# Kernel optimization log

Hardware: AMD Instinct MI355X
Metric: run time of the kernel (lower is better)

The kernel has to match this reference:

```python
import jax, jax.numpy as jnp
import numpy as np

EPS = 1e-5
B, C, N = 2, 256, 65536


def conv1x1(x, W, b):
    # Conv1d with kernel_size=1: (B,Cin,N) x (Cout,Cin) -> (B,Cout,N)
    return jnp.einsum('oc,bcn->bon', W, x) + b[None, :, None]


def instance_norm(x):
    # InstanceNorm1d, affine=False, biased variance over the spatial dim
    m = jnp.mean(x, axis=-1, keepdims=True)
    v = jnp.var(x, axis=-1, keepdims=True)
    return (x - m) * jax.lax.rsqrt(v + EPS)


def mesh_conv(x, gemm, W, b):
    # MeshCNN MeshConv: gather self + 4 one-ring neighbor edges, symmetric fns, (1,5) conv.
    Bb, Cc, E = x.shape
    xp = jnp.concatenate([jnp.zeros((Bb, Cc, 1), x.dtype), x], axis=2)  # pad slot 0 (for -1/missing)
    eid = jnp.broadcast_to(jnp.arange(E, dtype=gemm.dtype)[None, :, None], (Bb, E, 1))
    Gi = jnp.concatenate([eid, gemm], axis=2) + 1                      # (B,E,5), +1 shift for pad row
    xt = xp.transpose(0, 2, 1)                                          # (B,E+1,C)
    f = jax.vmap(lambda xb, gb: xb[gb])(xt, Gi)                         # (B,E,5,C) gather
    f = f.transpose(0, 3, 1, 2)                                         # (B,C,E,5)
    f0, f1, f2, f3, f4 = (f[..., i] for i in range(5))
    g = jnp.stack([f0, f1 + f3, f2 + f4, jnp.abs(f1 - f3), jnp.abs(f2 - f4)], axis=-1)
    # Conv2d(Cin,Cout,(1,5)) over (B,C,E,5) -> (B,Cout,E)
    return jnp.einsum('ock,bcek->boe', W, g) + b[None, :, None]


def setup_inputs() -> dict:
    key = jax.random.key(0)
    ks = jax.random.split(key, 20)
    s = 0.05
    inp = {
        'x_0': jax.random.normal(ks[0], (B, C, N), jnp.float32),
        'x_1': jax.random.normal(ks[1], (B, C, N), jnp.float32),
        'gemm': jax.random.randint(ks[2], (B, N, 4), 0, N, jnp.int32),
        # conv_a / conv_b: C -> C//4
        'Wa': jax.random.normal(ks[3], (C // 4, C), jnp.float32) * s,
        'ba': jax.random.normal(ks[4], (C // 4,), jnp.float32) * s,
        'Wb': jax.random.normal(ks[5], (C // 4, C), jnp.float32) * s,
        'bb': jax.random.normal(ks[6], (C // 4,), jnp.float32) * s,
        # conv_a_local / conv_b_local: C//2 -> C//2
        'Wal': jax.random.normal(ks[7], (C // 2, C // 2), jnp.float32) * s,
        'bal': jax.random.normal(ks[8], (C // 2,), jnp.float32) * s,
        'Wbl': jax.random.normal(ks[9], (C // 2, C // 2), jnp.float32) * s,
        'bbl': jax.random.normal(ks[10], (C // 2,), jnp.float32) * s,
        # MeshConv weights: (Cout, Cin, 5)
        'Wat': jax.random.normal(ks[11], (C // 2, C // 2, 5), jnp.float32) * s,
        'bat': jax.random.normal(ks[12], (C // 2,), jnp.float32) * s,
        'Wbt': jax.random.normal(ks[13], (C // 2, C // 2, 5), jnp.float32) * s,
        'bbt': jax.random.normal(ks[14], (C // 2,), jnp.float32) * s,
        # fuse convs: C -> C
        'Waf': jax.random.normal(ks[15], (C, C), jnp.float32) * s,
        'baf': jax.random.normal(ks[16], (C,), jnp.float32) * s,
        'Wbf': jax.random.normal(ks[17], (C, C), jnp.float32) * s,
        'bbf': jax.random.normal(ks[18], (C,), jnp.float32) * s,
    }
    return inp


def reference(x_0, x_1, gemm, Wa, ba, Wb, bb, Wal, bal, Wbl, bbl,
              Wat, bat, Wbt, bbt, Waf, baf, Wbf, bbf):
    x_a = conv1x1(x_0, Wa, ba)
    x_b = conv1x1(x_1, Wb, bb)
    x_all = jnp.concatenate([x_a, x_b], axis=1)          # (B, C/2, N)
    a_local = conv1x1(x_all, Wal, bal)
    a_tri = mesh_conv(x_all, gemm, Wat, bat)
    x_a_two = jnp.concatenate([a_local, a_tri], axis=1)  # (B, C, N)
    b_local = conv1x1(x_all, Wbl, bbl)
    b_tri = mesh_conv(x_all, gemm, Wbt, bbt)
    x_b_two = jnp.concatenate([b_local, b_tri], axis=1)
    wa = jax.nn.sigmoid(instance_norm(conv1x1(x_a_two, Waf, baf)))
    wb = jax.nn.sigmoid(instance_norm(conv1x1(x_b_two, Wbf, bbf)))
    w = jax.nn.softmax(jnp.stack([wa, wb], axis=1), axis=1)  # (B,2,C,N)
    return x_0 * w[:, 0] + x_1 * w[:, 1]
```

## Files before the change

kernel.cpp:

```cpp
#include <hip/hip_runtime.h>
#include <stdint.h>

#define NEDGE 65536

typedef __attribute__((ext_vector_type(4))) float f32x4;
typedef __attribute__((ext_vector_type(8))) __bf16 bf16x8;

#define VMCNT(n) asm volatile("s_waitcnt vmcnt(" #n ")" ::: "memory")
#define VMCNT_LGKM0(n) asm volatile("s_waitcnt vmcnt(" #n ") lgkmcnt(0)" ::: "memory")

__device__ __forceinline__ uint16_t f2bf(float f) {
  union { float f; uint32_t u; } v; v.f = f;
  uint32_t r = v.u + 0x7FFFu + ((v.u >> 16) & 1u);
  return (uint16_t)(r >> 16);
}
__device__ __forceinline__ float bflo(uint32_t u) {
  union { uint32_t u; float f; } v; v.u = u << 16; return v.f;
}
__device__ __forceinline__ float bfhi(uint32_t u) {
  union { uint32_t u; float f; } v; v.u = u & 0xFFFF0000u; return v.f;
}
__device__ __forceinline__ uint32_t packbf(float lo, float hi) {
  return (uint32_t)f2bf(lo) | ((uint32_t)f2bf(hi) << 16);
}
__device__ __forceinline__ void gload_lds16(const void* g, void* l) {
  __builtin_amdgcn_global_load_lds(
      (__attribute__((address_space(1))) uint32_t*)(uintptr_t)g,
      (__attribute__((address_space(3))) uint32_t*)l, 16, 0, 0);
}
__device__ __forceinline__ float sigm(float z) { return 1.0f / (1.0f + __expf(-z)); }

__global__ void k_compose(const float* __restrict__ Wal, const float* __restrict__ Wbl,
                          const float* __restrict__ Wat, const float* __restrict__ Wbt,
                          const float* __restrict__ Waf, const float* __restrict__ Wbf,
                          uint16_t* __restrict__ Wt) {
  int id = blockIdx.x * 256 + threadIdx.x;
  if (id >= 512 * 640) return;
  int j = id / 640, kk = id % 640;
  const float* Wf = (j < 256) ? Waf : Wbf;
  const float* Wl = (j < 256) ? Wal : Wbl;
  const float* Wr = (j < 256) ? Wat : Wbt;
  int jj = j & 255;
  float acc = 0.f;
  if (kk < 128) {
    int c = kk;
    for (int o = 0; o < 128; ++o) acc += Wl[o * 128 + c] * Wf[jj * 256 + o];
    for (int o = 0; o < 128; ++o) acc += Wr[(o * 128 + c) * 5 + 0] * Wf[jj * 256 + 128 + o];
  } else {
    int blkid = (kk - 128) >> 7;
    int gk = (blkid == 0) ? 1 : (blkid == 1) ? 3 : (blkid == 2) ? 2 : 4;
    int c = (kk - 128) & 127;
    for (int o = 0; o < 128; ++o) acc += Wr[(o * 128 + c) * 5 + gk] * Wf[jj * 256 + 128 + o];
  }
  Wt[j * 640 + kk] = f2bf(acc);
}

__global__ void k_bias(const float* __restrict__ bal, const float* __restrict__ bat,
                       const float* __restrict__ baf, const float* __restrict__ bbl,
                       const float* __restrict__ bbt, const float* __restrict__ bbf,
                       const float* __restrict__ Waf, const float* __restrict__ Wbf,
                       float* __restrict__ biasF) {
  int id = blockIdx.x * 256 + threadIdx.x;
  if (id >= 512) return;
  const float* Wf = (id < 256) ? Waf : Wbf;
  const float* bl = (id < 256) ? bal : bbl;
  const float* bt = (id < 256) ? bat : bbt;
  const float* bsf = (id < 256) ? baf : bbf;
  int jj = id & 255;
  float acc = bsf[jj];
  for (int o = 0; o < 128; ++o) acc += Wf[jj * 256 + o] * bl[o];
  for (int o = 0; o < 128; ++o) acc += Wf[jj * 256 + 128 + o] * bt[o];
  biasF[id] = acc;
}

__global__ void k_wt1(const float* __restrict__ Wa, const float* __restrict__ Wb,
                      uint16_t* __restrict__ W1bf) {
  int id = blockIdx.x * 256 + threadIdx.x;
  if (id >= 2 * 64 * 256) return;
  int side = id >> 14, r = id & 16383;
  W1bf[id] = f2bf(side ? Wb[r] : Wa[r]);
}

__global__ __launch_bounds__(256) void k1_xa(
    const float* __restrict__ x0, const float* __restrict__ x1,
    const uint16_t* __restrict__ W1bf, const float* __restrict__ ba,
    const float* __restrict__ bb, uint16_t* __restrict__ XA) {
  __shared__ __align__(16) float Xs[3][32 * 128];
  __shared__ __align__(16) uint16_t Bs[64 * 256];
  int t = threadIdx.x;
  int side = blockIdx.y, b = blockIdx.z;
  int n0 = blockIdx.x * 128;
  const float* xin = (side ? x1 : x0) + (size_t)b * 256 * NEDGE + n0;
  const uint16_t* wsrc = W1bf + side * 64 * 256;

#pragma unroll
  for (int q = 0; q < 8; ++q) {
    int s = q * 256 + t;
    int j = s >> 5, pb = s & 31;
    int lb = pb ^ (j & 7);
    gload_lds16(wsrc + j * 256 + lb * 8, &Bs[s * 8]);
  }
#pragma unroll
  for (int c = 0; c < 2; ++c) {
#pragma unroll
    for (int q = 0; q < 4; ++q) {
      int s = q * 256 + t;
      int cl = s >> 5, pb = s & 31;
      int lb = pb ^ (((cl >> 3) & 3) << 2);
      gload_lds16(xin + (size_t)(c * 32 + cl) * NEDGE + lb * 4, &Xs[c][s * 4]);
    }
  }

  int wv = t >> 6, l = t & 63;
  int m = l & 15, g = l >> 4;
  int pcol[2];
#pragma unroll
  for (int nf = 0; nf < 2; ++nf) {
    int n = wv * 32 + nf * 16 + m;
    pcol[nf] = (((n >> 2) ^ (g << 2)) << 2) + (n & 3);
  }

  f32x4 acc[2][4];
  f32x4 zero = {0.f, 0.f, 0.f, 0.f};
#pragma unroll
  for (int nf = 0; nf < 2; ++nf)
#pragma unroll
    for (int jf = 0; jf < 4; ++jf) acc[nf][jf] = zero;

#pragma unroll
  for (int ks = 0; ks < 8; ++ks) {
    if (ks < 6) {
      const float* xc = xin + (size_t)(ks + 2) * 32 * NEDGE;
#pragma unroll
      for (int q = 0; q < 4; ++q) {
        int s = q * 256 + t;
        int cl = s >> 5, pb = s & 31;
        int lb = pb ^ (((cl >> 3) & 3) << 2);
        gload_lds16(xc + (size_t)cl * NEDGE + lb * 4, &Xs[(ks + 2) % 3][s * 4]);
      }
      VMCNT(8);
    } else if (ks == 6) {
      VMCNT(4);
    } else {
      VMCNT(0);
    }
    __builtin_amdgcn_sched_barrier(0);
    __builtin_amdgcn_s_barrier();

    const float* Xb = Xs[ks % 3];
    bf16x8 af[4];
#pragma unroll
    for (int jf = 0; jf < 4; ++jf) {
      int jloc = jf * 16 + m;
      int pbb = (ks * 4 + g) ^ (jloc & 7);
      af[jf] = *(const bf16x8*)&Bs[jloc * 256 + pbb * 8];
    }
#pragma unroll
    for (int nf = 0; nf < 2; ++nf) {
      const float* base = Xb + g * 8 * 128 + pcol[nf];
      float xv[8];
#pragma unroll
      for (int i = 0; i < 8; ++i) xv[i] = base[i * 128];
      union { bf16x8 v; uint32_t u[4]; } bx;
      bx.u[0] = packbf(xv[0], xv[1]);
      bx.u[1] = packbf(xv[2], xv[3]);
      bx.u[2] = packbf(xv[4], xv[5]);
      bx.u[3] = packbf(xv[6], xv[7]);
#pragma unroll
      for (int jf = 0; jf < 4; ++jf)
        acc[nf][jf] = __builtin_amdgcn_mfma_f32_16x16x32_bf16(af[jf], bx.v, acc[nf][jf], 0, 0, 0);
    }
    __builtin_amdgcn_s_barrier();
  }

  const float* bias = side ? bb : ba;
  uint16_t* XAb = XA + (size_t)b * NEDGE * 128;
#pragma unroll
  for (int jf = 0; jf < 4; ++jf) {
    f32x4 bv = *(const f32x4*)(bias + jf * 16 + g * 4);
#pragma unroll
    for (int nf = 0; nf < 2; ++nf) {
      int n = n0 + wv * 32 + nf * 16 + m;
      uint2 o;
      o.x = packbf(acc[nf][jf][0] + bv[0], acc[nf][jf][1] + bv[1]);
      o.y = packbf(acc[nf][jf][2] + bv[2], acc[nf][jf][3] + bv[3]);
      *(uint2*)(XAb + (size_t)n * 128 + side * 64 + jf * 16 + g * 4) = o;
    }
  }
}

__global__ __launch_bounds__(512) void k23_gemm(
    const uint16_t* __restrict__ XAb, const int* __restrict__ gidx,
    const uint16_t* __restrict__ Wt, const float* __restrict__ biasF,
    uint16_t* __restrict__ Y, float* __restrict__ part) {
  __shared__ __align__(16) uint16_t As[2][128 * 64];
  __shared__ __align__(16) uint16_t Bs2[2][256 * 64];
  __shared__ int gi[512];
  __shared__ float sL[2][256][2];
  int t = threadIdx.x;
  int jbase = blockIdx.x * 256;
  int bx = blockIdx.y;
  int ebase = bx * 128;
  int wid = t >> 6, lane = t & 63;
  int wr = wid >> 2, wc = wid & 3;
  int m = lane & 15, g = lane >> 4;

  gi[t] = gidx[(size_t)ebase * 4 + t];
  __syncthreads();

  const int r0 = t >> 3, cc = t & 7;
  int iP13[2], iQ13[2], iP24[2], iQ24[2];
#pragma unroll
  for (int q2 = 0; q2 < 2; ++q2) {
    int r = r0 + q2 * 64;
    iP13[q2] = gi[r * 4 + 0]; iQ13[q2] = gi[r * 4 + 2];
    iP24[q2] = gi[r * 4 + 1]; iQ24[q2] = gi[r * 4 + 3];
  }

  uint4 grP[2][2], grQ[2][2];

#define ISSUE_GATH(v)                                                           \
  do {                                                                          \
    const int coffv = ((v) & 1) * 64;                                           \
    const int pr = ((v) - 2) >> 2;              \
    _Pragma("unroll")                                                           \
    for (int q2 = 0; q2 < 2; ++q2) {                                            \
      int ip = pr ? iP24[q2] : iP13[q2];                                        \
      int iq = pr ? iQ24[q2] : iQ13[q2];                                        \
      grP[(v) & 1][q2] = *(const uint4*)(XAb + (size_t)ip * 128 + coffv + cc * 8); \
      grQ[(v) & 1][q2] = *(const uint4*)(XAb + (size_t)iq * 128 + coffv + cc * 8); \
    }                                                                           \
  } while (0)

#define ISSUE_BS(s_)                                                            \
  do {                                                                          \
    _Pragma("unroll")                                                           \
    for (int q = 0; q < 4; ++q) {                                               \
      int slot = q * 512 + t; int r = slot >> 3, c16 = slot & 7;                \
      gload_lds16(Wt + (size_t)(jbase + r) * 640 + (s_) * 64 + (c16 ^ (r & 7)) * 8, \
                  &Bs2[(s_) & 1][slot * 8]);                                    \
    }                                                                           \
  } while (0)

#define ISSUE_AS_DIRECT(s_)                                                     \
  do {                                                                          \
    _Pragma("unroll")                                                           \
    for (int q = 0; q < 2; ++q) {                                               \
      int slot = q * 512 + t; int r = slot >> 3, c16 = slot & 7;                \
      gload_lds16(XAb + (size_t)(ebase + r) * 128 + (s_) * 64 + (c16 ^ (r & 7)) * 8, \
                  &As[(s_) & 1][slot * 8]);                                     \
    }                                                                           \
  } while (0)

  ISSUE_GATH(2);
  ISSUE_AS_DIRECT(0);
  ISSUE_BS(0);
  ISSUE_AS_DIRECT(1);
  ISSUE_BS(1);

  f32x4 acc[4][4];
  f32x4 zero = {0.f, 0.f, 0.f, 0.f};
#pragma unroll
  for (int r = 0; r < 4; ++r)
#pragma unroll
    for (int c = 0; c < 4; ++c) acc[r][c] = zero;

#pragma unroll
  for (int u = 0; u < 10; ++u) {
    const int su = u + 1;
    if (su >= 2 && su <= 9) {
      if (u == 1) { VMCNT(6); } else { VMCNT(4); }
      const int sum_op = (((su - 2) >> 1) & 1) == 0;
      const int bi = su & 1;
#pragma unroll
      for (int q2 = 0; q2 < 2; ++q2) {
        int r = r0 + q2 * 64;
        uint4 P = grP[bi][q2], Q = grQ[bi][q2];
        uint4 R;
        if (sum_op) {
          R.x = packbf(bflo(P.x) + bflo(Q.x), bfhi(P.x) + bfhi(Q.x));
          R.y = packbf(bflo(P.y) + bflo(Q.y), bfhi(P.y) + bfhi(Q.y));
          R.z = packbf(bflo(P.z) + bflo(Q.z), bfhi(P.z) + bfhi(Q.z));
          R.w = packbf(bflo(P.w) + bflo(Q.w), bfhi(P.w) + bfhi(Q.w));
        } else {
          R.x = packbf(fabsf(bflo(P.x) - bflo(Q.x)), fabsf(bfhi(P.x) - bfhi(Q.x)));
          R.y = packbf(fabsf(bflo(P.y) - bflo(Q.y)), fabsf(bfhi(P.y) - bfhi(Q.y)));
          R.z = packbf(fabsf(bflo(P.z) - bflo(Q.z)), fabsf(bfhi(P.z) - bfhi(Q.z)));
          R.w = packbf(fabsf(bflo(P.w) - bflo(Q.w)), fabsf(bfhi(P.w) - bfhi(Q.w)));
        }
        *(uint4*)&As[bi][(r * 8 + (cc ^ (r & 7))) * 8] = R;
      }
    }
    if (u + 2 >= 3 && u + 2 <= 9) ISSUE_GATH(u + 2);
    if (su >= 2 && su <= 9) ISSUE_BS(su);
    if (u == 0) { VMCNT_LGKM0(6); }
    else if (u <= 7) { VMCNT_LGKM0(8); }
    else if (u == 8) { VMCNT_LGKM0(4); }
    else { VMCNT_LGKM0(0); }
    __builtin_amdgcn_sched_barrier(0);
    __builtin_amdgcn_s_barrier();

    const uint16_t* Ab = As[u & 1];
    const uint16_t* Bb = Bs2[u & 1];
#pragma unroll
    for (int kit = 0; kit < 2; ++kit) {
      bf16x8 af[4], bf[4];
#pragma unroll
      for (int r = 0; r < 4; ++r) {
        int row = wr * 64 + r * 16 + m;
        af[r] = *(const bf16x8*)&Ab[row * 64 + ((kit * 4 + g) ^ (m & 7)) * 8];
      }
#pragma unroll
      for (int cf = 0; cf < 4; ++cf) {
        int row = wc * 64 + cf * 16 + m;
        bf[cf] = *(const bf16x8*)&Bb[row * 64 + ((kit * 4 + g) ^ (m & 7)) * 8];
      }
#pragma unroll
      for (int r = 0; r < 4; ++r)
#pragma unroll
        for (int cf = 0; cf < 4; ++cf)
          acc[r][cf] = __builtin_amdgcn_mfma_f32_16x16x32_bf16(bf[cf], af[r], acc[r][cf], 0, 0, 0);
    }
    __builtin_amdgcn_s_barrier();
  }
#undef ISSUE_GATH
#undef ISSUE_BS
#undef ISSUE_AS_DIRECT

  float s1[4][4], s2[4][4];
#pragma unroll
  for (int cf = 0; cf < 4; ++cf)
#pragma unroll
    for (int q = 0; q < 4; ++q) { s1[cf][q] = 0.f; s2[cf][q] = 0.f; }

#pragma unroll
  for (int cf = 0; cf < 4; ++cf) {
    f32x4 bv = *(const f32x4*)(biasF + jbase + wc * 64 + cf * 16 + g * 4);
#pragma unroll
    for (int r = 0; r < 4; ++r) {
      int eg = ebase + wr * 64 + r * 16 + m;
      float v0 = acc[r][cf][0] + bv[0];
      float v1 = acc[r][cf][1] + bv[1];
      float v2 = acc[r][cf][2] + bv[2];
      float v3 = acc[r][cf][3] + bv[3];
      s1[cf][0] += v0; s2[cf][0] += v0 * v0;
      s1[cf][1] += v1; s2[cf][1] += v1 * v1;
      s1[cf][2] += v2; s2[cf][2] += v2 * v2;
      s1[cf][3] += v3; s2[cf][3] += v3 * v3;
      uint2 o;
      o.x = packbf(v0, v1);
      o.y = packbf(v2, v3);
      *(uint2*)(Y + (size_t)eg * 512 + jbase + wc * 64 + cf * 16 + g * 4) = o;
    }
  }
#pragma unroll
  for (int cf = 0; cf < 4; ++cf)
#pragma unroll
    for (int q = 0; q < 4; ++q) {
#pragma unroll
      for (int off = 1; off < 16; off <<= 1) {
        s1[cf][q] += __shfl_xor(s1[cf][q], off);
        s2[cf][q] += __shfl_xor(s2[cf][q], off);
      }
    }
  if (m == 0) {
#pragma unroll
    for (int cf = 0; cf < 4; ++cf)
#pragma unroll
      for (int q = 0; q < 4; ++q) {
        int jl = wc * 64 + cf * 16 + g * 4 + q;
        sL[wr][jl][0] = s1[cf][q];
        sL[wr][jl][1] = s2[cf][q];
      }
  }
  __syncthreads();
  if (t < 256) {
    float a1 = sL[0][t][0] + sL[1][t][0];
    float a2 = sL[0][t][1] + sL[1][t][1];
    float* p = part + ((size_t)bx * 512 + jbase + t) * 2;
    p[0] = a1; p[1] = a2;
  }
}

__global__ void k3b2(const float* __restrict__ part, float* __restrict__ statF) {
  int col = blockIdx.x, t = threadIdx.x;
  float s1 = 0, s2 = 0;
  for (int k = t; k < 512; k += 128) {
    const float* p = part + ((size_t)k * 512 + col) * 2;
    s1 += p[0]; s2 += p[1];
  }
  for (int off = 32; off; off >>= 1) { s1 += __shfl_down(s1, off); s2 += __shfl_down(s2, off); }
  __shared__ float sh[4];
  if ((t & 63) == 0) { sh[(t >> 6) * 2] = s1; sh[(t >> 6) * 2 + 1] = s2; }
  __syncthreads();
  if (t == 0) {
    s1 = sh[0] + sh[2]; s2 = sh[1] + sh[3];
    float mean = s1 * (1.0f / 65536.0f);
    float var = s2 * (1.0f / 65536.0f) - mean * mean;
    statF[col * 2] = mean;
    statF[col * 2 + 1] = rsqrtf(var + 1e-5f);
  }
}

__global__ __launch_bounds__(256) void k4_final(
    const uint16_t* __restrict__ Y, const float* __restrict__ statF,
    const float* __restrict__ x0b, const float* __restrict__ x1b,
    float* __restrict__ outb) {
  __shared__ float W0[128][65];
  __shared__ float mA[128], rA[128], mB[128], rB[128];
  int t = threadIdx.x;
  int n0 = blockIdx.x * 64;
  int ch = blockIdx.y;
  if (t < 128) {
    mA[t] = statF[(ch * 128 + t) * 2];
    rA[t] = statF[(ch * 128 + t) * 2 + 1];
  } else {
    int q = t - 128;
    mB[q] = statF[(256 + ch * 128 + q) * 2];
    rB[q] = statF[(256 + ch * 128 + q) * 2 + 1];
  }
  __syncthreads();
  const char* Ybase = (const char*)Y;
  for (int i = t; i < 64 * 64; i += 256) {
    int row = i >> 6, cp = i & 63;
    const char* yr = Ybase + (size_t)(n0 + row) * 1024;
    uint32_t ya2 = *(const uint32_t*)(yr + ch * 256 + cp * 4);
    uint32_t yb2 = *(const uint32_t*)(yr + 512 + ch * 256 + cp * 4);
    int c0 = 2 * cp, c1 = 2 * cp + 1;
    float wa0 = sigm((bflo(ya2) - mA[c0]) * rA[c0]);
    float wa1 = sigm((bfhi(ya2) - mA[c1]) * rA[c1]);
    float wb0 = sigm((bflo(yb2) - mB[c0]) * rB[c0]);
    float wb1 = sigm((bfhi(yb2) - mB[c1]) * rB[c1]);
    W0[c0][row] = sigm(wa0 - wb0);
    W0[c1][row] = sigm(wa1 - wb1);
  }
  __syncthreads();
  int nn = t & 63, cg = t >> 6;
  for (int cc = cg; cc < 128; cc += 4) {
    int c = ch * 128 + cc;
    size_t gi = (size_t)c * NEDGE + n0 + nn;
    float w0 = W0[cc][nn];
    outb[gi] = x0b[gi] * w0 + x1b[gi] * (1.0f - w0);
  }
}

extern "C" void kernel_launch(void* const* d_in, const int* in_sizes, int n_in,
                              void* d_out, int out_size, void* d_ws, size_t ws_size,
                              hipStream_t stream) {
  const float* x0 = (const float*)d_in[0];
  const float* x1 = (const float*)d_in[1];
  const int* gemm = (const int*)d_in[2];
  const float* Wa = (const float*)d_in[3];
  const float* ba = (const float*)d_in[4];
  const float* Wb = (const float*)d_in[5];
  const float* bb = (const float*)d_in[6];
  const float* Wal = (const float*)d_in[7];
  const float* bal = (const float*)d_in[8];
  const float* Wbl = (const float*)d_in[9];
  const float* bbl = (const float*)d_in[10];
  const float* Wat = (const float*)d_in[11];
  const float* bat = (const float*)d_in[12];
  const float* Wbt = (const float*)d_in[13];
  const float* bbt = (const float*)d_in[14];
  const float* Waf = (const float*)d_in[15];
  const float* baf = (const float*)d_in[16];
  const float* Wbf = (const float*)d_in[17];
  const float* bbf = (const float*)d_in[18];
  float* out = (float*)d_out;

  char* ws = (char*)d_ws;
  uint16_t* XA   = (uint16_t*)ws;
  uint16_t* Yb   = (uint16_t*)(ws + 33554432);
  uint16_t* Wt   = (uint16_t*)(ws + 100663296);
  uint16_t* W1bf = (uint16_t*)(ws + 101318656);
  float*    biasF= (float*)(ws + 101384192);
  float*    part = (float*)(ws + 101386240);
  float*    statF= (float*)(ws + 103483392);

  k_compose<<<dim3(1280), dim3(256), 0, stream>>>(Wal, Wbl, Wat, Wbt, Waf, Wbf, Wt);
  k_bias<<<dim3(2), dim3(256), 0, stream>>>(bal, bat, baf, bbl, bbt, bbf, Waf, Wbf, biasF);
  k_wt1<<<dim3(128), dim3(256), 0, stream>>>(Wa, Wb, W1bf);
  k1_xa<<<dim3(512, 2, 2), dim3(256), 0, stream>>>(x0, x1, W1bf, ba, bb, XA);

  for (int b = 0; b < 2; ++b) {
    const uint16_t* XAb = XA + (size_t)b * NEDGE * 128;
    k23_gemm<<<dim3(2, 512), dim3(512), 0, stream>>>(
        XAb, gemm + (size_t)b * NEDGE * 4, Wt, biasF, Yb, part);
    k3b2<<<dim3(512), dim3(128), 0, stream>>>(part, statF + b * 1024);
    k4_final<<<dim3(1024, 2), dim3(256), 0, stream>>>(
        Yb, statF + b * 1024, x0 + (size_t)b * 256 * NEDGE,
        x1 + (size_t)b * 256 * NEDGE, out + (size_t)b * 256 * NEDGE);
  }
}
```

Measured before the change: 412.6 us.

## Load GEMM weight fragments directly into registers instead of staging in LDS

In both k1_xa and k23_gemm, the weight tiles are no longer staged through shared memory. Each lane now loads its MFMA A-fragment straight from global memory with global_load_dwordx4, and the waitcnt schedule is reworked to match. k23_gemm also preloads both direct XA slices up front and single-buffers the gather registers, and occupancy hints are added to the launch bounds. This cuts LDS footprint and LDS traffic so more blocks can be resident, at the cost of redundant per-wave global loads of the weights and a shallower gather prefetch.

New measurement: 770.1 us. 1.87x slower.

```diff
diff --git a/kernel.cpp b/kernel.cpp
--- a/kernel.cpp
+++ b/kernel.cpp
@@ -7,7 +7,8 @@
 typedef __attribute__((ext_vector_type(8))) __bf16 bf16x8;
 
 #define VMCNT(n) asm volatile("s_waitcnt vmcnt(" #n ")" ::: "memory")
-#define VMCNT_LGKM0(n) asm volatile("s_waitcnt vmcnt(" #n ") lgkmcnt(0)" ::: "memory")
+#define LGKM0 asm volatile("s_waitcnt lgkmcnt(0)" ::: "memory")
+#define SCHEDB __builtin_amdgcn_sched_barrier(0)
 
 __device__ __forceinline__ uint16_t f2bf(float f) {
   union { float f; uint32_t u; } v; v.f = f;
@@ -27,6 +28,11 @@
   __builtin_amdgcn_global_load_lds(
       (__attribute__((address_space(1))) uint32_t*)(uintptr_t)g,
       (__attribute__((address_space(3))) uint32_t*)l, 16, 0, 0);
+}
+__device__ __forceinline__ uint4 gload16(const void* p) {
+  uint4 d;
+  asm volatile("global_load_dwordx4 %0, %1, off" : "=v"(d) : "v"(p));
+  return d;
 }
 __device__ __forceinline__ float sigm(float z) { return 1.0f / (1.0f + __expf(-z)); }
 
@@ -81,25 +87,29 @@
   W1bf[id] = f2bf(side ? Wb[r] : Wa[r]);
 }
 
-__global__ __launch_bounds__(256) void k1_xa(
+__global__ __launch_bounds__(256, 3) void k1_xa(
     const float* __restrict__ x0, const float* __restrict__ x1,
     const uint16_t* __restrict__ W1bf, const float* __restrict__ ba,
     const float* __restrict__ bb, uint16_t* __restrict__ XA) {
   __shared__ __align__(16) float Xs[3][32 * 128];
-  __shared__ __align__(16) uint16_t Bs[64 * 256];
   int t = threadIdx.x;
   int side = blockIdx.y, b = blockIdx.z;
   int n0 = blockIdx.x * 128;
   const float* xin = (side ? x1 : x0) + (size_t)b * 256 * NEDGE + n0;
   const uint16_t* wsrc = W1bf + side * 64 * 256;
 
-#pragma unroll
-  for (int q = 0; q < 8; ++q) {
-    int s = q * 256 + t;
-    int j = s >> 5, pb = s & 31;
-    int lb = pb ^ (j & 7);
-    gload_lds16(wsrc + j * 256 + lb * 8, &Bs[s * 8]);
-  }
+  int wv = t >> 6, l = t & 63;
+  int m = l & 15, g = l >> 4;
+  const uint16_t* wjb[4];
+#pragma unroll
+  for (int jf = 0; jf < 4; ++jf) wjb[jf] = wsrc + (jf * 16 + m) * 256 + g * 8;
+  int pcol[2];
+#pragma unroll
+  for (int nf = 0; nf < 2; ++nf) {
+    int n = wv * 32 + nf * 16 + m;
+    pcol[nf] = (((n >> 2) ^ (g << 2)) << 2) + (n & 3);
+  }
+
 #pragma unroll
   for (int c = 0; c < 2; ++c) {
 #pragma unroll
@@ -111,15 +121,6 @@
     }
   }
 
-  int wv = t >> 6, l = t & 63;
-  int m = l & 15, g = l >> 4;
-  int pcol[2];
-#pragma unroll
-  for (int nf = 0; nf < 2; ++nf) {
-    int n = wv * 32 + nf * 16 + m;
-    pcol[nf] = (((n >> 2) ^ (g << 2)) << 2) + (n & 3);
-  }
-
   f32x4 acc[2][4];
   f32x4 zero = {0.f, 0.f, 0.f, 0.f};
 #pragma unroll
@@ -129,6 +130,9 @@
 
 #pragma unroll
   for (int ks = 0; ks < 8; ++ks) {
+    uint4 wt[4];
+#pragma unroll
+    for (int jf = 0; jf < 4; ++jf) wt[jf] = gload16(wjb[jf] + ks * 32);
     if (ks < 6) {
       const float* xc = xin + (size_t)(ks + 2) * 32 * NEDGE;
 #pragma unroll
@@ -138,23 +142,18 @@
         int lb = pb ^ (((cl >> 3) & 3) << 2);
         gload_lds16(xc + (size_t)cl * NEDGE + lb * 4, &Xs[(ks + 2) % 3][s * 4]);
       }
-      VMCNT(8);
-    } else if (ks == 6) {
-      VMCNT(4);
-    } else {
-      VMCNT(0);
-    }
-    __builtin_amdgcn_sched_barrier(0);
+    }
+    if (ks < 6) { VMCNT(8); } else if (ks == 6) { VMCNT(4); }
+    SCHEDB;
     __builtin_amdgcn_s_barrier();
-
+    SCHEDB;
+    if (ks < 6) { VMCNT(4); } else { VMCNT(0); }
+    SCHEDB;
+
+    union { uint4 u; bf16x8 v; } afu[4];
+#pragma unroll
+    for (int jf = 0; jf < 4; ++jf) afu[jf].u = wt[jf];
     const float* Xb = Xs[ks % 3];
-    bf16x8 af[4];
-#pragma unroll
-    for (int jf = 0; jf < 4; ++jf) {
-      int jloc = jf * 16 + m;
-      int pbb = (ks * 4 + g) ^ (jloc & 7);
-      af[jf] = *(const bf16x8*)&Bs[jloc * 256 + pbb * 8];
-    }
 #pragma unroll
     for (int nf = 0; nf < 2; ++nf) {
       const float* base = Xb + g * 8 * 128 + pcol[nf];
@@ -168,9 +167,11 @@
       bx.u[3] = packbf(xv[6], xv[7]);
 #pragma unroll
       for (int jf = 0; jf < 4; ++jf)
-        acc[nf][jf] = __builtin_amdgcn_mfma_f32_16x16x32_bf16(af[jf], bx.v, acc[nf][jf], 0, 0, 0);
-    }
+        acc[nf][jf] = __builtin_amdgcn_mfma_f32_16x16x32_bf16(afu[jf].v, bx.v, acc[nf][jf], 0, 0, 0);
+    }
+    LGKM0;
     __builtin_amdgcn_s_barrier();
+    SCHEDB;
   }
 
   const float* bias = side ? bb : ba;
@@ -189,12 +190,11 @@
   }
 }
 
-__global__ __launch_bounds__(512) void k23_gemm(
+__global__ __launch_bounds__(512, 4) void k23_gemm(
     const uint16_t* __restrict__ XAb, const int* __restrict__ gidx,
     const uint16_t* __restrict__ Wt, const float* __restrict__ biasF,
     uint16_t* __restrict__ Y, float* __restrict__ part) {
   __shared__ __align__(16) uint16_t As[2][128 * 64];
-  __shared__ __align__(16) uint16_t Bs2[2][256 * 64];
   __shared__ int gi[512];
   __shared__ float sL[2][256][2];
   int t = threadIdx.x;
@@ -206,6 +206,17 @@
   int m = lane & 15, g = lane >> 4;
 
   gi[t] = gidx[(size_t)ebase * 4 + t];
+#pragma unroll
+  for (int s = 0; s < 2; ++s) {
+#pragma unroll
+    for (int q = 0; q < 2; ++q) {
+      int slot = q * 512 + t;
+      int r = slot >> 3, c16 = slot & 7;
+      gload_lds16(XAb + (size_t)(ebase + r) * 128 + s * 64 + (c16 ^ (r & 7)) * 8,
+                  &As[s][slot * 8]);
+    }
+  }
+  VMCNT(0);
   __syncthreads();
 
   const int r0 = t >> 3, cc = t & 7;
@@ -216,47 +227,12 @@
     iP13[q2] = gi[r * 4 + 0]; iQ13[q2] = gi[r * 4 + 2];
     iP24[q2] = gi[r * 4 + 1]; iQ24[q2] = gi[r * 4 + 3];
   }
-
-  uint4 grP[2][2], grQ[2][2];
-
-#define ISSUE_GATH(v)                                                           \
-  do {                                                                          \
-    const int coffv = ((v) & 1) * 64;                                           \
-    const int pr = ((v) - 2) >> 2;              \
-    _Pragma("unroll")                                                           \
-    for (int q2 = 0; q2 < 2; ++q2) {                                            \
-      int ip = pr ? iP24[q2] : iP13[q2];                                        \
-      int iq = pr ? iQ24[q2] : iQ13[q2];                                        \
-      grP[(v) & 1][q2] = *(const uint4*)(XAb + (size_t)ip * 128 + coffv + cc * 8); \
-      grQ[(v) & 1][q2] = *(const uint4*)(XAb + (size_t)iq * 128 + coffv + cc * 8); \
-    }                                                                           \
-  } while (0)
-
-#define ISSUE_BS(s_)                                                            \
-  do {                                                                          \
-    _Pragma("unroll")                                                           \
-    for (int q = 0; q < 4; ++q) {                                               \
-      int slot = q * 512 + t; int r = slot >> 3, c16 = slot & 7;                \
-      gload_lds16(Wt + (size_t)(jbase + r) * 640 + (s_) * 64 + (c16 ^ (r & 7)) * 8, \
-                  &Bs2[(s_) & 1][slot * 8]);                                    \
-    }                                                                           \
-  } while (0)
-
-#define ISSUE_AS_DIRECT(s_)                                                     \
-  do {                                                                          \
-    _Pragma("unroll")                                                           \
-    for (int q = 0; q < 2; ++q) {                                               \
-      int slot = q * 512 + t; int r = slot >> 3, c16 = slot & 7;                \
-      gload_lds16(XAb + (size_t)(ebase + r) * 128 + (s_) * 64 + (c16 ^ (r & 7)) * 8, \
-                  &As[(s_) & 1][slot * 8]);                                     \
-    }                                                                           \
-  } while (0)
-
-  ISSUE_GATH(2);
-  ISSUE_AS_DIRECT(0);
-  ISSUE_BS(0);
-  ISSUE_AS_DIRECT(1);
-  ISSUE_BS(1);
+  const uint16_t* wbase[4];
+#pragma unroll
+  for (int cf = 0; cf < 4; ++cf)
+    wbase[cf] = Wt + (size_t)(jbase + wc * 64 + cf * 16 + m) * 640 + g * 8;
+
+  uint4 grP[2], grQ[2];
 
   f32x4 acc[4][4];
   f32x4 zero = {0.f, 0.f, 0.f, 0.f};
@@ -267,15 +243,15 @@
 
 #pragma unroll
   for (int u = 0; u < 10; ++u) {
-    const int su = u + 1;
-    if (su >= 2 && su <= 9) {
-      if (u == 1) { VMCNT(6); } else { VMCNT(4); }
-      const int sum_op = (((su - 2) >> 1) & 1) == 0;
-      const int bi = su & 1;
+    if (u >= 1 && u <= 8) {
+      VMCNT(0);
+      SCHEDB;
+      const int su = u + 1;
+      const bool sum_op = (((su - 2) >> 1) & 1) == 0;
 #pragma unroll
       for (int q2 = 0; q2 < 2; ++q2) {
         int r = r0 + q2 * 64;
-        uint4 P = grP[bi][q2], Q = grQ[bi][q2];
+        uint4 P = grP[q2], Q = grQ[q2];
         uint4 R;
         if (sum_op) {
           R.x = packbf(bflo(P.x) + bflo(Q.x), bfhi(P.x) + bfhi(Q.x));
@@ -288,44 +264,67 @@
           R.z = packbf(fabsf(bflo(P.z) - bflo(Q.z)), fabsf(bfhi(P.z) - bfhi(Q.z)));
           R.w = packbf(fabsf(bflo(P.w) - bflo(Q.w)), fabsf(bfhi(P.w) - bfhi(Q.w)));
         }
-        *(uint4*)&As[bi][(r * 8 + (cc ^ (r & 7))) * 8] = R;
-      }
-    }
-    if (u + 2 >= 3 && u + 2 <= 9) ISSUE_GATH(u + 2);
-    if (su >= 2 && su <= 9) ISSUE_BS(su);
-    if (u == 0) { VMCNT_LGKM0(6); }
-    else if (u <= 7) { VMCNT_LGKM0(8); }
-    else if (u == 8) { VMCNT_LGKM0(4); }
-    else { VMCNT_LGKM0(0); }
-    __builtin_amdgcn_sched_barrier(0);
-    __builtin_amdgcn_s_barrier();
-
-    const uint16_t* Ab = As[u & 1];
-    const uint16_t* Bb = Bs2[u & 1];
-#pragma unroll
-    for (int kit = 0; kit < 2; ++kit) {
-      bf16x8 af[4], bf[4];
+        *(uint4*)&As[su & 1][(r * 8 + (cc ^ (r & 7))) * 8] = R;
+      }
+    }
+    uint4 wt0[4], wt1[4];
+#pragma unroll
+    for (int cf = 0; cf < 4; ++cf) wt0[cf] = gload16(wbase[cf] + u * 64);
+#pragma unroll
+    for (int cf = 0; cf < 4; ++cf) wt1[cf] = gload16(wbase[cf] + u * 64 + 32);
+    if (u <= 7) {
+      const int v = u + 2;
+      const int coffv = (v & 1) * 64;
+      const int pr = (v - 2) >> 2;
+#pragma unroll
+      for (int q2 = 0; q2 < 2; ++q2) {
+        int ip = pr ? iP24[q2] : iP13[q2];
+        int iq = pr ? iQ24[q2] : iQ13[q2];
+        grP[q2] = gload16(XAb + (size_t)ip * 128 + coffv + cc * 8);
+        grQ[q2] = gload16(XAb + (size_t)iq * 128 + coffv + cc * 8);
+      }
+    }
+    SCHEDB;
+    {
+      bf16x8 af[4];
 #pragma unroll
       for (int r = 0; r < 4; ++r) {
         int row = wr * 64 + r * 16 + m;
-        af[r] = *(const bf16x8*)&Ab[row * 64 + ((kit * 4 + g) ^ (m & 7)) * 8];
-      }
+        af[r] = *(const bf16x8*)&As[u & 1][row * 64 + ((0 * 4 + g) ^ (m & 7)) * 8];
+      }
+      if (u <= 7) { VMCNT(8); } else { VMCNT(4); }
+      SCHEDB;
+      union { uint4 u4; bf16x8 v; } w;
 #pragma unroll
       for (int cf = 0; cf < 4; ++cf) {
-        int row = wc * 64 + cf * 16 + m;
-        bf[cf] = *(const bf16x8*)&Bb[row * 64 + ((kit * 4 + g) ^ (m & 7)) * 8];
-      }
-#pragma unroll
-      for (int r = 0; r < 4; ++r)
-#pragma unroll
-        for (int cf = 0; cf < 4; ++cf)
-          acc[r][cf] = __builtin_amdgcn_mfma_f32_16x16x32_bf16(bf[cf], af[r], acc[r][cf], 0, 0, 0);
-    }
+        w.u4 = wt0[cf];
+#pragma unroll
+        for (int r = 0; r < 4; ++r)
+          acc[r][cf] = __builtin_amdgcn_mfma_f32_16x16x32_bf16(w.v, af[r], acc[r][cf], 0, 0, 0);
+      }
+    }
+    {
+      bf16x8 af[4];
+#pragma unroll
+      for (int r = 0; r < 4; ++r) {
+        int row = wr * 64 + r * 16 + m;
+        af[r] = *(const bf16x8*)&As[u & 1][row * 64 + ((1 * 4 + g) ^ (m & 7)) * 8];
+      }
+      if (u <= 7) { VMCNT(4); } else { VMCNT(0); }
+      SCHEDB;
+      union { uint4 u4; bf16x8 v; } w;
+#pragma unroll
+      for (int cf = 0; cf < 4; ++cf) {
+        w.u4 = wt1[cf];
+#pragma unroll
+        for (int r = 0; r < 4; ++r)
+          acc[r][cf] = __builtin_amdgcn_mfma_f32_16x16x32_bf16(w.v, af[r], acc[r][cf], 0, 0, 0);
+      }
+    }
+    LGKM0;
     __builtin_amdgcn_s_barrier();
-  }
-#undef ISSUE_GATH
-#undef ISSUE_BS
-#undef ISSUE_AS_DIRECT
+    SCHEDB;
+  }
 
   float s1[4][4], s2[4][4];
 #pragma unroll
@@ -436,11 +435,11 @@
   }
   __syncthreads();
   int nn = t & 63, cg = t >> 6;
-  for (int cc = cg; cc < 128; cc += 4) {
-    int c = ch * 128 + cc;
-    size_t gi = (size_t)c * NEDGE + n0 + nn;
-    float w0 = W0[cc][nn];
-    outb[gi] = x0b[gi] * w0 + x1b[gi] * (1.0f - w0);
+  for (int cc2 = cg; cc2 < 128; cc2 += 4) {
+    int c = ch * 128 + cc2;
+    size_t gidx2 = (size_t)c * NEDGE + n0 + nn;
+    float w0 = W0[cc2][nn];
+    outb[gidx2] = x0b[gidx2] * w0 + x1b[gidx2] * (1.0f - w0);
   }
 }
 
```

## Single-buffer weight tile and shrink gather pipeline to fit two blocks per CU

Applied to the files above, without the earlier changes.

The mesh-conv GEMM kernel drops the double-buffered weight tile in LDS and the double-buffered gather registers, and declares launch bounds asking for two 512-thread blocks per CU. The prologue now loads both A slabs up front, and each step issues the weight load for the current stage and waits on it in the same step. The aim is more resident waves to hide gather latency. In exchange, each step now waits on its own weight load and has less prefetch depth. Extra sched barriers and an lgkmcnt wait are added around the barriers in the first kernel.

Result: slower. 425.1 us (+3.1%).

```diff
diff --git a/kernel.cpp b/kernel.cpp
--- a/kernel.cpp
+++ b/kernel.cpp
@@ -7,7 +7,8 @@
 typedef __attribute__((ext_vector_type(8))) __bf16 bf16x8;
 
 #define VMCNT(n) asm volatile("s_waitcnt vmcnt(" #n ")" ::: "memory")
-#define VMCNT_LGKM0(n) asm volatile("s_waitcnt vmcnt(" #n ") lgkmcnt(0)" ::: "memory")
+#define LGKM0 asm volatile("s_waitcnt lgkmcnt(0)" ::: "memory")
+#define SCHEDB __builtin_amdgcn_sched_barrier(0)
 
 __device__ __forceinline__ uint16_t f2bf(float f) {
   union { float f; uint32_t u; } v; v.f = f;
@@ -144,8 +145,9 @@
     } else {
       VMCNT(0);
     }
-    __builtin_amdgcn_sched_barrier(0);
+    SCHEDB;
     __builtin_amdgcn_s_barrier();
+    SCHEDB;
 
     const float* Xb = Xs[ks % 3];
     bf16x8 af[4];
@@ -170,7 +172,9 @@
       for (int jf = 0; jf < 4; ++jf)
         acc[nf][jf] = __builtin_amdgcn_mfma_f32_16x16x32_bf16(af[jf], bx.v, acc[nf][jf], 0, 0, 0);
     }
+    LGKM0;
     __builtin_amdgcn_s_barrier();
+    SCHEDB;
   }
 
   const float* bias = side ? bb : ba;
@@ -189,12 +193,12 @@
   }
 }
 
-__global__ __launch_bounds__(512) void k23_gemm(
+__global__ __launch_bounds__(512, 2) void k23_gemm(
     const uint16_t* __restrict__ XAb, const int* __restrict__ gidx,
     const uint16_t* __restrict__ Wt, const float* __restrict__ biasF,
     uint16_t* __restrict__ Y, float* __restrict__ part) {
   __shared__ __align__(16) uint16_t As[2][128 * 64];
-  __shared__ __align__(16) uint16_t Bs2[2][256 * 64];
+  __shared__ __align__(16) uint16_t Bs[256 * 64];
   __shared__ int gi[512];
   __shared__ float sL[2][256][2];
   int t = threadIdx.x;
@@ -206,31 +210,6 @@
   int m = lane & 15, g = lane >> 4;
 
   gi[t] = gidx[(size_t)ebase * 4 + t];
-  __syncthreads();
-
-  const int r0 = t >> 3, cc = t & 7;
-  int iP13[2], iQ13[2], iP24[2], iQ24[2];
-#pragma unroll
-  for (int q2 = 0; q2 < 2; ++q2) {
-    int r = r0 + q2 * 64;
-    iP13[q2] = gi[r * 4 + 0]; iQ13[q2] = gi[r * 4 + 2];
-    iP24[q2] = gi[r * 4 + 1]; iQ24[q2] = gi[r * 4 + 3];
-  }
-
-  uint4 grP[2][2], grQ[2][2];
-
-#define ISSUE_GATH(v)                                                           \
-  do {                                                                          \
-    const int coffv = ((v) & 1) * 64;                                           \
-    const int pr = ((v) - 2) >> 2;              \
-    _Pragma("unroll")                                                           \
-    for (int q2 = 0; q2 < 2; ++q2) {                                            \
-      int ip = pr ? iP24[q2] : iP13[q2];                                        \
-      int iq = pr ? iQ24[q2] : iQ13[q2];                                        \
-      grP[(v) & 1][q2] = *(const uint4*)(XAb + (size_t)ip * 128 + coffv + cc * 8); \
-      grQ[(v) & 1][q2] = *(const uint4*)(XAb + (size_t)iq * 128 + coffv + cc * 8); \
-    }                                                                           \
-  } while (0)
 
 #define ISSUE_BS(s_)                                                            \
   do {                                                                          \
@@ -238,25 +217,47 @@
     for (int q = 0; q < 4; ++q) {                                               \
       int slot = q * 512 + t; int r = slot >> 3, c16 = slot & 7;                \
       gload_lds16(Wt + (size_t)(jbase + r) * 640 + (s_) * 64 + (c16 ^ (r & 7)) * 8, \
-                  &Bs2[(s_) & 1][slot * 8]);                                    \
+                  &Bs[slot * 8]);                                               \
     }                                                                           \
   } while (0)
 
-#define ISSUE_AS_DIRECT(s_)                                                     \
+#pragma unroll
+  for (int s = 0; s < 2; ++s) {
+#pragma unroll
+    for (int q = 0; q < 2; ++q) {
+      int slot = q * 512 + t;
+      int r = slot >> 3, c16 = slot & 7;
+      gload_lds16(XAb + (size_t)(ebase + r) * 128 + s * 64 + (c16 ^ (r & 7)) * 8,
+                  &As[s][slot * 8]);
+    }
+  }
+  ISSUE_BS(0);
+  __syncthreads();
+
+  const int r0 = t >> 3, cc = t & 7;
+  int iP13[2], iQ13[2], iP24[2], iQ24[2];
+#pragma unroll
+  for (int q2 = 0; q2 < 2; ++q2) {
+    int r = r0 + q2 * 64;
+    iP13[q2] = gi[r * 4 + 0]; iQ13[q2] = gi[r * 4 + 2];
+    iP24[q2] = gi[r * 4 + 1]; iQ24[q2] = gi[r * 4 + 3];
+  }
+
+  uint4 grP[2], grQ[2];
+#define ISSUE_GATH(v)                                                           \
   do {                                                                          \
+    const int coffv = ((v) & 1) * 64;                                           \
+    const int pr = ((v) - 2) >> 2;                                              \
     _Pragma("unroll")                                                           \
-    for (int q = 0; q < 2; ++q) {                                               \
-      int slot = q * 512 + t; int r = slot >> 3, c16 = slot & 7;                \
-      gload_lds16(XAb + (size_t)(ebase + r) * 128 + (s_) * 64 + (c16 ^ (r & 7)) * 8, \
-                  &As[(s_) & 1][slot * 8]);                                     \
+    for (int q2 = 0; q2 < 2; ++q2) {                                            \
+      int ip = pr ? iP24[q2] : iP13[q2];                                        \
+      int iq = pr ? iQ24[q2] : iQ13[q2];                                        \
+      grP[q2] = *(const uint4*)(XAb + (size_t)ip * 128 + coffv + cc * 8);       \
+      grQ[q2] = *(const uint4*)(XAb + (size_t)iq * 128 + coffv + cc * 8);       \
     }                                                                           \
   } while (0)
 
   ISSUE_GATH(2);
-  ISSUE_AS_DIRECT(0);
-  ISSUE_BS(0);
-  ISSUE_AS_DIRECT(1);
-  ISSUE_BS(1);
 
   f32x4 acc[4][4];
   f32x4 zero = {0.f, 0.f, 0.f, 0.f};
@@ -267,15 +268,16 @@
 
 #pragma unroll
   for (int u = 0; u < 10; ++u) {
-    const int su = u + 1;
-    if (su >= 2 && su <= 9) {
-      if (u == 1) { VMCNT(6); } else { VMCNT(4); }
-      const int sum_op = (((su - 2) >> 1) & 1) == 0;
-      const int bi = su & 1;
+    if (u >= 1) ISSUE_BS(u);
+    if (u >= 1 && u <= 8) {
+      VMCNT(4);
+      SCHEDB;
+      const int su = u + 1;
+      const bool sum_op = (((su - 2) >> 1) & 1) == 0;
 #pragma unroll
       for (int q2 = 0; q2 < 2; ++q2) {
         int r = r0 + q2 * 64;
-        uint4 P = grP[bi][q2], Q = grQ[bi][q2];
+        uint4 P = grP[q2], Q = grQ[q2];
         uint4 R;
         if (sum_op) {
           R.x = packbf(bflo(P.x) + bflo(Q.x), bfhi(P.x) + bfhi(Q.x));
@@ -288,20 +290,17 @@
           R.z = packbf(fabsf(bflo(P.z) - bflo(Q.z)), fabsf(bfhi(P.z) - bfhi(Q.z)));
           R.w = packbf(fabsf(bflo(P.w) - bflo(Q.w)), fabsf(bfhi(P.w) - bfhi(Q.w)));
         }
-        *(uint4*)&As[bi][(r * 8 + (cc ^ (r & 7))) * 8] = R;
-      }
-    }
-    if (u + 2 >= 3 && u + 2 <= 9) ISSUE_GATH(u + 2);
-    if (su >= 2 && su <= 9) ISSUE_BS(su);
-    if (u == 0) { VMCNT_LGKM0(6); }
-    else if (u <= 7) { VMCNT_LGKM0(8); }
-    else if (u == 8) { VMCNT_LGKM0(4); }
-    else { VMCNT_LGKM0(0); }
-    __builtin_amdgcn_sched_barrier(0);
+        *(uint4*)&As[su & 1][(r * 8 + (cc ^ (r & 7))) * 8] = R;
+      }
+    }
+    if (u >= 1 && u <= 7) ISSUE_GATH(u + 2);
+    if (u <= 7) { VMCNT(4); } else { VMCNT(0); }
+    LGKM0;
+    SCHEDB;
     __builtin_amdgcn_s_barrier();
+    SCHEDB;
 
     const uint16_t* Ab = As[u & 1];
-    const uint16_t* Bb = Bs2[u & 1];
 #pragma unroll
     for (int kit = 0; kit < 2; ++kit) {
       bf16x8 af[4], bf[4];
@@ -313,7 +312,7 @@
 #pragma unroll
       for (int cf = 0; cf < 4; ++cf) {
         int row = wc * 64 + cf * 16 + m;
-        bf[cf] = *(const bf16x8*)&Bb[row * 64 + ((kit * 4 + g) ^ (m & 7)) * 8];
+        bf[cf] = *(const bf16x8*)&Bs[row * 64 + ((kit * 4 + g) ^ (m & 7)) * 8];
       }
 #pragma unroll
       for (int r = 0; r < 4; ++r)
@@ -322,10 +321,10 @@
           acc[r][cf] = __builtin_amdgcn_mfma_f32_16x16x32_bf16(bf[cf], af[r], acc[r][cf], 0, 0, 0);
     }
     __builtin_amdgcn_s_barrier();
+    SCHEDB;
   }
 #undef ISSUE_GATH
 #undef ISSUE_BS
-#undef ISSUE_AS_DIRECT
 
   float s1[4][4], s2[4][4];
 #pragma unroll
@@ -436,11 +435,11 @@
   }
   __syncthreads();
   int nn = t & 63, cg = t >> 6;
-  for (int cc = cg; cc < 128; cc += 4) {
-    int c = ch * 128 + cc;
-    size_t gi = (size_t)c * NEDGE + n0 + nn;
-    float w0 = W0[cc][nn];
-    outb[gi] = x0b[gi] * w0 + x1b[gi] * (1.0f - w0);
+  for (int cc2 = cg; cc2 < 128; cc2 += 4) {
+    int c = ch * 128 + cc2;
+    size_t gidx2 = (size_t)c * NEDGE + n0 + nn;
+    float w0 = W0[cc2][nn];
+    outb[gidx2] = x0b[gidx2] * w0 + x1b[gidx2] * (1.0f - w0);
   }
 }
 
```
